# Kernel optimization log

Hardware: AMD Instinct MI355X
Metric: run time of the kernel (lower is better)

Reference implementation:

```python
import jax, jax.numpy as jnp
import numpy as np

NUM_COEFF = 32   # num_coeff_per_dim
NUM_POINTS = 64  # Chebyshev collocation points
MAX_ITERS = 10
TOL = 0.01
BATCH, DIM, HID, T_EVAL_N = 512, 256, 512, 16


def T_grid(t, n):
    # Chebyshev T_k(t), k=0..n-1 -> [n, len(t)]
    rows = [jnp.ones_like(t), t]
    for _ in range(2, n):
        rows.append(2.0 * t * rows[-1] - rows[-2])
    return jnp.stack(rows[:n])


def U_grid(t, n):
    rows = [jnp.ones_like(t), 2.0 * t]
    for _ in range(2, n):
        rows.append(2.0 * t * rows[-1] - rows[-2])
    return jnp.stack(rows[:n])


def DT_grid(t, n):
    # d/dt T_k = k * U_{k-1}
    return jnp.vstack([jnp.zeros((1, t.shape[0]), t.dtype),
                       U_grid(t, n - 1) * jnp.arange(1, n, dtype=t.dtype)[:, None]])


def vf_point(t, y, W1, b1, W2, b2):
    # f(t, y) for y [B, D], scalar t
    h = jnp.tanh(y @ W1 + b1 + t)
    return h @ W2 + b2


def vf_grid(t, y, W1, b1, W2, b2):
    # vectorized over Chebyshev points: y [B, D, P], t [P]
    h = jnp.tanh(jnp.einsum('bdp,dh->bhp', y, W1) + b1[None, :, None] + t[None, None, :])
    return jnp.einsum('bhp,hd->bdp', h, W2) + b2[None, :, None]


def setup_inputs() -> dict:
    key = jax.random.key(0)
    ks = jax.random.split(key, 7)
    s1 = 1.0 / np.sqrt(DIM)
    s2 = 1.0 / np.sqrt(HID)
    return {
        'y_init': jax.random.normal(ks[0], (BATCH, DIM), jnp.float32),
        't_eval': jnp.linspace(0.0, 1.0, T_EVAL_N, dtype=jnp.float32),
        'B_init': jax.random.uniform(ks[1], (BATCH, DIM, NUM_COEFF - 2), jnp.float32),
        'W1': jax.random.normal(ks[2], (DIM, HID), jnp.float32) * s1,
        'b1': jax.random.normal(ks[3], (HID,), jnp.float32) * 0.1,
        'W2': jax.random.normal(ks[4], (HID, DIM), jnp.float32) * s2,
        'b2': jax.random.normal(ks[5], (DIM,), jnp.float32) * 0.1,
    }


def _pan_solve(y_init, t_eval, B_init, W1, b1, W2, b2):
    t0, t1 = t_eval[0], t_eval[-1]
    dt = t_eval.dtype
    # time-independent spectral operators
    t_cheb = -jnp.sign(t1 - t0) * jnp.cos(jnp.pi * jnp.arange(NUM_POINTS, dtype=dt) / NUM_POINTS)
    Dt = jnp.diff(jnp.concatenate([t_cheb, jnp.ones((1,), dt)]))
    Phi = T_grid(t_cheb, NUM_COEFF)                        # [N, P]
    DPhi = (2.0 / (t1 - t0)) * DT_grid(t_cheb, NUM_COEFF)  # [N, P]
    inv0 = jnp.linalg.inv(jnp.stack([Phi[0:2, 0], DPhi[0:2, 0]]).T)  # [2,2]
    PD2 = jnp.stack([Phi[2:, 0], DPhi[2:, 0]], axis=-1)    # [N-2, 2]
    D01 = jnp.stack([DPhi[0, :], DPhi[1, :]], axis=0)      # [2, P]
    Phi_b = DPhi[2:, :] - PD2 @ inv0 @ D01                 # [N-2, P]
    Q = jnp.linalg.inv(Phi_b @ (Dt[:, None] * Phi_b.T))    # [N-2, N-2]
    PhibTQ = (Dt[:, None] * Phi_b.T) @ Q                   # [P, N-2]
    M2 = inv0 @ D01 @ PhibTQ                               # [2, N-2]

    f_init = vf_point(t0, y_init, W1, b1, W2, b2)
    yf2 = jnp.stack([y_init, f_init], axis=-1)             # [B, D, 2]

    def head(B_tail):
        return (yf2 - B_tail @ PD2) @ inv0                 # [B, D, 2]

    B = B_init
    done = jnp.array(False)
    delta = jnp.array(jnp.inf, dt)
    iters = jnp.array(0, jnp.int32)
    for _ in range(MAX_ITERS):  # Picard fixed-point iteration (masked early stop)
        B_prev = B
        B_full = jnp.concatenate([head(B_prev), B_prev], axis=-1)  # [B, D, N]
        y_grid = jnp.einsum('bdn,np->bdp', B_full, Phi)            # [B, D, P]
        fapprox = vf_grid(t_cheb, y_grid, W1, b1, W2, b2)          # [B, D, P]
        B_new = jnp.einsum('bdp,pn->bdn', fapprox, PhibTQ) - yf2 @ M2
        d = jnp.linalg.norm(B_new - B_prev)
        B = jnp.where(done, B_prev, B_new)
        delta = jnp.where(done, delta, d)
        iters = jnp.where(done, iters, iters + 1)
        done = done | (d < TOL)

    B_full = jnp.concatenate([head(B), B], axis=-1)
    t_out = -1.0 + 2.0 * (t_eval - t0) / (t1 - t0)
    Phi_out = T_grid(t_out, NUM_COEFF)                     # [N, T]
    traj = jnp.einsum('bdn,nt->tbd', B_full, Phi_out)      # [T, B, D]
    return traj, B, delta, iters


def reference(y_init, t_eval, B_init, W1, b1, W2, b2):
    traj, B, delta, iters = _pan_solve(y_init, t_eval, B_init, W1, b1, W2, b2)
    return (t_eval, traj, delta, B)
```

## Files before the change

kernel.cpp:

```cpp
#include <hip/hip_runtime.h>
#include <math.h>

#define NBATCH 512
#define NDIM 256
#define NHID 512
#define NC 32
#define NTAIL 30
#define NP 64
#define TEV 16
#define MAXIT 10
#define TOLF 0.01f
#define PI_F 3.14159265358979323846f

typedef __bf16 bf16_t;
typedef __bf16 bf16x8 __attribute__((ext_vector_type(8)));
typedef float f32x4 __attribute__((ext_vector_type(4)));
typedef unsigned short ushort_t;

constexpr size_t OFF_TCHEB = 0;
constexpr size_t OFF_PHIT  = 64;
constexpr size_t OFF_PD2I  = 2112;
constexpr size_t OFF_M2    = 2176;
constexpr size_t OFF_INV0  = 2240;
constexpr size_t OFF_PHIOUT= 2256;
constexpr size_t OFF_PQ    = 2768;
constexpr size_t OFF_PQBH  = 4816;
constexpr size_t OFF_PQBL  = 5840;
constexpr size_t OFF_PHIH  = 6864;
constexpr size_t OFF_PHIL  = 7888;
constexpr size_t OFF_SCAL  = 8912;
constexpr size_t OFF_H1F   = 8928;
constexpr size_t OFF_YF2I  = OFF_H1F + 262144;
constexpr size_t OFF_YM2   = OFF_YF2I + 262144;
constexpr size_t OFF_BT    = OFF_YM2 + 3932160;
constexpr size_t OFF_W1T   = OFF_BT + 3932160;
constexpr size_t OFF_W2T   = OFF_W1T + 65536;
constexpr size_t WS_FLOATS = OFF_W2T + 65536;

constexpr size_t OUT_TEVAL = 0;
constexpr size_t OUT_TRAJ  = 16;
constexpr size_t OUT_DELTA = 16 + (size_t)TEV*NBATCH*NDIM;
constexpr size_t OUT_B     = OUT_DELTA + 1;

__device__ __forceinline__ ushort_t bf16bits(float v) {
    bf16_t h = (bf16_t)v; ushort_t u; __builtin_memcpy(&u, &h, 2); return u;
}
__device__ __forceinline__ float bf16val(ushort_t u) {
    bf16_t h; __builtin_memcpy(&h, &u, 2); return (float)h;
}

__global__ void setup_kernel(const float* __restrict__ t_eval, float* __restrict__ ws,
                             float* __restrict__ out)
{
    __shared__ float Phi[32][64];
    __shared__ float DPhi[32][64];
    __shared__ float Phib[30][64];
    __shared__ float tcs[64];
    __shared__ float DtS[64];
    __shared__ float inv0s[4];
    __shared__ float pd2s[30][2];
    __shared__ double Gaug[30][61];
    __shared__ double rowk[60];
    __shared__ double colk[30];

    const int tid = threadIdx.x;
    const float t0 = t_eval[0], t1 = t_eval[TEV-1];
    const float sgn = (t1 > t0) ? 1.f : -1.f;

    if (tid < 64) {
        const float t = -sgn * cosf(PI_F * (float)tid / 64.f);
        tcs[tid] = t;
        float p0 = 1.f, p1 = t;
        Phi[0][tid] = p0; Phi[1][tid] = p1;
        for (int k = 2; k < 32; ++k) { float pk = 2.f*t*p1 - p0; Phi[k][tid] = pk; p0 = p1; p1 = pk; }
        const float sc = 2.f / (t1 - t0);
        float u0 = 1.f, u1 = 2.f*t;
        DPhi[0][tid] = 0.f;
        DPhi[1][tid] = sc * 1.f * u0;
        DPhi[2][tid] = sc * 2.f * u1;
        for (int k = 3; k < 32; ++k) { float uk = 2.f*t*u1 - u0; DPhi[k][tid] = sc * (float)k * uk; u0 = u1; u1 = uk; }
    }
    __syncthreads();
    if (tid < 64) DtS[tid] = ((tid < 63) ? tcs[tid+1] : 1.0f) - tcs[tid];
    if (tid == 0) {
        double a = Phi[0][0], b = DPhi[0][0], c = Phi[1][0], d = DPhi[1][0];
        double det = a*d - b*c;
        inv0s[0] = (float)( d/det); inv0s[1] = (float)(-b/det);
        inv0s[2] = (float)(-c/det); inv0s[3] = (float)( a/det);
    }
    __syncthreads();
    if (tid == 0) { ws[OFF_INV0+0]=inv0s[0]; ws[OFF_INV0+1]=inv0s[1]; ws[OFF_INV0+2]=inv0s[2]; ws[OFF_INV0+3]=inv0s[3]; }
    if (tid < 30) {
        float P = Phi[2+tid][0], D = DPhi[2+tid][0];
        float a0 = P*inv0s[0] + D*inv0s[2];
        float a1 = P*inv0s[1] + D*inv0s[3];
        pd2s[tid][0] = a0; pd2s[tid][1] = a1;
        ws[OFF_PD2I + tid*2+0] = a0;
        ws[OFF_PD2I + tid*2+1] = a1;
    }
    __syncthreads();
    if (tid < 64)
        for (int m = 0; m < 30; ++m)
            Phib[m][tid] = DPhi[2+m][tid] - (pd2s[m][0]*DPhi[0][tid] + pd2s[m][1]*DPhi[1][tid]);
    __syncthreads();

    for (int e = tid; e < 900; e += 256) {
        int i = e / 30, j = e % 30;
        double s = 0.0;
        for (int p = 0; p < 64; ++p) s += (double)Phib[i][p] * (double)DtS[p] * (double)Phib[j][p];
        Gaug[i][j] = s;
        Gaug[i][30+j] = (i == j) ? 1.0 : 0.0;
    }
    __syncthreads();

    for (int k = 0; k < 30; ++k) {
        double invpv = 1.0 / Gaug[k][k];
        if (tid < 60) rowk[tid] = Gaug[k][tid] * invpv;
        if (tid >= 64 && tid < 94) colk[tid-64] = Gaug[tid-64][k];
        __syncthreads();
        for (int e = tid; e < 1800; e += 256) {
            int i = e / 60, j = e - i*60;
            if (i == k) Gaug[i][j] = rowk[j];
            else        Gaug[i][j] -= colk[i] * rowk[j];
        }
        __syncthreads();
    }

    if (tid < 64) {
        ushort_t* pqh = (ushort_t*)(ws + OFF_PQBH);
        ushort_t* pql = (ushort_t*)(ws + OFF_PQBL);
        float pqrow[32];
        for (int n = 0; n < 30; ++n) {
            double s = 0.0;
            for (int m = 0; m < 30; ++m) s += (double)Phib[m][tid] * Gaug[m][30+n];
            pqrow[n] = (float)((double)DtS[tid] * s);
        }
        pqrow[30] = 0.f; pqrow[31] = 0.f;
        for (int n = 0; n < 32; ++n) {
            ws[OFF_PQ + (size_t)tid*32 + n] = pqrow[n];
            bf16_t h = (bf16_t)pqrow[n];
            float hf = (float)h;
            pqh[n*64 + tid] = bf16bits(pqrow[n]);
            pql[n*64 + tid] = bf16bits(pqrow[n] - hf);
        }
    }
    __syncthreads();

    if (tid < 30) {
        double a20 = 0.0, a21 = 0.0;
        for (int p = 0; p < 64; ++p) {
            double pq = (double)ws[OFF_PQ + (size_t)p*32 + tid];
            a20 += (double)DPhi[0][p] * pq;
            a21 += (double)DPhi[1][p] * pq;
        }
        ws[OFF_M2 + 0*32 + tid] = (float)((double)inv0s[0]*a20 + (double)inv0s[1]*a21);
        ws[OFF_M2 + 1*32 + tid] = (float)((double)inv0s[2]*a20 + (double)inv0s[3]*a21);
    }

    if (tid < 64) {
        ushort_t* phh = (ushort_t*)(ws + OFF_PHIH);
        ushort_t* phl = (ushort_t*)(ws + OFF_PHIL);
        for (int n = 0; n < 32; ++n) {
            float f = Phi[n][tid];
            ws[OFF_PHIT + (size_t)tid*32 + n] = f;
            ushort_t hb = bf16bits(f);
            phh[tid*32 + n] = hb;
            phl[tid*32 + n] = bf16bits(f - bf16val(hb));
        }
        ws[OFF_TCHEB + tid] = tcs[tid];
    }

    if (tid < TEV) {
        float te = t_eval[tid];
        out[OUT_TEVAL + tid] = te;
        float tt = -1.f + 2.f*(te - t0)/(t1 - t0);
        float q0 = 1.f, q1 = tt;
        ws[OFF_PHIOUT + (size_t)tid*32 + 0] = q0;
        ws[OFF_PHIOUT + (size_t)tid*32 + 1] = q1;
        for (int k = 2; k < 32; ++k) { float qk = 2.f*tt*q1 - q0; ws[OFF_PHIOUT + (size_t)tid*32 + k] = qk; q0 = q1; q1 = qk; }
    }

    if (tid == 0) {
        double* acc = (double*)(ws + OFF_SCAL);
        acc[0] = 0.0;
        int* ip = (int*)(ws + OFF_SCAL + 2);
        ip[0] = 0;
        ip[1] = 0;
    }
}

__global__ __launch_bounds__(256) void transB_kernel(const float* __restrict__ Bin, float* __restrict__ Bt)
{
    const int t = threadIdx.x, b = blockIdx.x;
    const float* src = Bin + ((size_t)(b*NDIM + t)) * NTAIL;
    #pragma unroll
    for (int n = 0; n < NTAIL; ++n)
        Bt[((size_t)b*NTAIL + n)*NDIM + t] = src[n];
}

__global__ __launch_bounds__(256) void transW_kernel(const float* __restrict__ W, bf16_t* __restrict__ Wt,
                                                     int R, int C)
{
    __shared__ float Ls[64][65];
    const int r0 = blockIdx.x*64, c0 = blockIdx.y*64;
    const int lr = threadIdx.x >> 6, lc = threadIdx.x & 63;
    #pragma unroll
    for (int i = 0; i < 16; ++i) {
        int rr = i*4 + lr;
        Ls[rr][lc] = W[(size_t)(r0+rr)*C + c0+lc];
    }
    __syncthreads();
    #pragma unroll
    for (int i = 0; i < 16; ++i) {
        int cc = i*4 + lr;
        Wt[(size_t)(c0+cc)*R + r0 + lc] = (bf16_t)Ls[lc][cc];
    }
}

__global__ __launch_bounds__(512) void finit_h_kernel(const float* __restrict__ y, const float* __restrict__ W1,
                                                      const float* __restrict__ b1, const float* __restrict__ t_eval,
                                                      float* __restrict__ h1)
{
    __shared__ float ys[NDIM];
    const int t = threadIdx.x, b = blockIdx.x;
    if (t < NDIM) ys[t] = y[(size_t)b*NDIM + t];
    __syncthreads();
    float acc = b1[t] + t_eval[0];
    for (int d = 0; d < NDIM; ++d) acc += ys[d] * W1[(size_t)d*NHID + t];
    h1[(size_t)b*NHID + t] = tanhf(acc);
}

__global__ __launch_bounds__(256) void finit_rest_kernel(const float* __restrict__ y, const float* __restrict__ W2,
                                                         const float* __restrict__ b2, const float* __restrict__ h1,
                                                         const float* __restrict__ inv0, const float* __restrict__ M2,
                                                         float* __restrict__ yf2i, float* __restrict__ yM2)
{
    __shared__ float hs[NHID];
    const int t = threadIdx.x, b = blockIdx.x;
    hs[t] = h1[(size_t)b*NHID + t];
    hs[t+256] = h1[(size_t)b*NHID + 256 + t];
    __syncthreads();
    float f = b2[t];
    for (int h = 0; h < NHID; ++h) f += hs[h] * W2[(size_t)h*NDIM + t];
    const float yv = y[(size_t)b*NDIM + t];
    yf2i[((size_t)b*2 + 0)*NDIM + t] = yv*inv0[0] + f*inv0[2];
    yf2i[((size_t)b*2 + 1)*NDIM + t] = yv*inv0[1] + f*inv0[3];
    #pragma unroll
    for (int n = 0; n < NTAIL; ++n)
        yM2[((size_t)b*NTAIL + n)*NDIM + t] = yv*M2[n] + f*M2[32 + n];
}

__global__ __launch_bounds__(256, 2) void iter_kernel(
    const float* __restrict__ pd2i, const float* __restrict__ yf2i, const float* __restrict__ tch,
    const bf16_t* __restrict__ W1t, const bf16_t* __restrict__ W2t,
    const float* __restrict__ b1f, const float* __restrict__ b2f,
    const ushort_t* __restrict__ PQhi, const ushort_t* __restrict__ PQlo,
    const ushort_t* __restrict__ phiH, const ushort_t* __restrict__ phiL,
    const float* __restrict__ yM2, float* __restrict__ Bt,
    double* __restrict__ accum, int* __restrict__ counter,
    int* __restrict__ done, float* __restrict__ outDelta)
{
    if (*done) return;
    __shared__ float pd2s[32][2];
    __shared__ float tchS[64];
    __shared__ double redd[4];
    __shared__ __align__(16) char smemA[33792];
    __shared__ __align__(16) char smemB[17408];
    __shared__ __align__(16) ushort_t PQHs[32*72];
    __shared__ __align__(16) ushort_t PQLs[32*72];

    const int t = threadIdx.x;
    const int b = blockIdx.x;
    const int lane = t & 63, w = t >> 6;
    const int fr = lane & 15, quad = lane >> 4;

    if (t < 60) ((float*)pd2s)[t] = pd2i[t];
    if (t >= 64 && t < 128) tchS[t-64] = tch[t-64];
    {
        int e = t * 8;
        int r = e >> 6, c = e & 63;
        uint4 vh = *(const uint4*)(PQhi + e);
        uint4 vl = *(const uint4*)(PQlo + e);
        *(uint4*)(PQHs + r*72 + c) = vh;
        *(uint4*)(PQLs + r*72 + c) = vl;
    }

    {
        float cf[32];
        #pragma unroll
        for (int n = 0; n < NTAIL; ++n) cf[2+n] = Bt[((size_t)b*NTAIL + n)*NDIM + t];
        float c0 = yf2i[((size_t)b*2 + 0)*NDIM + t];
        float c1 = yf2i[((size_t)b*2 + 1)*NDIM + t];
        #pragma unroll
        for (int n = 0; n < NTAIL; ++n) { c0 -= cf[2+n]*pd2s[n][0]; c1 -= cf[2+n]*pd2s[n][1]; }
        cf[0] = c0; cf[1] = c1;
        unsigned* BH32 = (unsigned*)smemA;
        unsigned* BL32 = (unsigned*)(smemA + 16384);
        #pragma unroll
        for (int n2 = 0; n2 < 16; ++n2) {
            float f0 = cf[2*n2], f1 = cf[2*n2+1];
            ushort_t h0 = bf16bits(f0), h1 = bf16bits(f1);
            ushort_t l0 = bf16bits(f0 - bf16val(h0)), l1 = bf16bits(f1 - bf16val(h1));
            int idx = t*16 + ((n2 >> 2) ^ (t & 3))*4 + (n2 & 3);
            BH32[idx] = (unsigned)h0 | ((unsigned)h1 << 16);
            BL32[idx] = (unsigned)l0 | ((unsigned)l1 << 16);
        }
    }
    __syncthreads();

    ushort_t* Ay = (ushort_t*)smemA;
    {
        bf16x8 bH[4], bL[4];
        const ushort_t* BHu = (const ushort_t*)smemA;
        const ushort_t* BLu = (const ushort_t*)(smemA + 16384);
        #pragma unroll
        for (int j = 0; j < 4; ++j) {
            const int d = w*64 + j*16 + fr;
            const int off = d*32 + (quad ^ (d & 3))*8;
            bH[j] = *(const bf16x8*)(BHu + off);
            bL[j] = *(const bf16x8*)(BLu + off);
        }
        bf16x8 aH[4], aL[4];
        #pragma unroll
        for (int i = 0; i < 4; ++i) {
            aH[i] = *(const bf16x8*)(phiH + (i*16 + fr)*32 + quad*8);
            aL[i] = *(const bf16x8*)(phiL + (i*16 + fr)*32 + quad*8);
        }
        __syncthreads();
        f32x4 accY[4][4];
        #pragma unroll
        for (int i = 0; i < 4; ++i)
            #pragma unroll
            for (int j = 0; j < 4; ++j) {
                f32x4 a = (f32x4){0.f,0.f,0.f,0.f};
                a = __builtin_amdgcn_mfma_f32_16x16x32_bf16(aH[i], bH[j], a, 0, 0, 0);
                a = __builtin_amdgcn_mfma_f32_16x16x32_bf16(aH[i], bL[j], a, 0, 0, 0);
                a = __builtin_amdgcn_mfma_f32_16x16x32_bf16(aL[i], bH[j], a, 0, 0, 0);
                accY[i][j] = a;
            }
        #pragma unroll
        for (int i = 0; i < 4; ++i)
            #pragma unroll
            for (int j = 0; j < 4; ++j)
                #pragma unroll
                for (int r = 0; r < 4; ++r) {
                    const int p = i*16 + quad*4 + r;
                    const int d = w*64 + j*16 + fr;
                    Ay[p*264 + d] = bf16bits(accY[i][j][r]);
                }
    }
    __syncthreads();

    ushort_t* Hc = (ushort_t*)smemB;
    f32x4 accF[4][4];
    #pragma unroll
    for (int i = 0; i < 4; ++i)
        #pragma unroll
        for (int j = 0; j < 4; ++j) accF[i][j] = (f32x4){0.f,0.f,0.f,0.f};

    #pragma unroll
    for (int pass = 0; pass < 4; ++pass) {
        f32x4 acc1[4][2];
        #pragma unroll
        for (int i = 0; i < 4; ++i)
            #pragma unroll
            for (int j = 0; j < 2; ++j) acc1[i][j] = (f32x4){0.f,0.f,0.f,0.f};
        #pragma unroll 2
        for (int kt = 0; kt < NDIM; kt += 32) {
            bf16x8 af[4], bfj[2];
            #pragma unroll
            for (int i = 0; i < 4; ++i)
                af[i] = *(const bf16x8*)(Ay + (i*16 + fr)*264 + kt + quad*8);
            #pragma unroll
            for (int j = 0; j < 2; ++j) {
                const int ncol = pass*128 + w*32 + j*16 + fr;
                bfj[j] = *(const bf16x8*)(W1t + (size_t)ncol*NDIM + kt + quad*8);
            }
            #pragma unroll
            for (int i = 0; i < 4; ++i)
                #pragma unroll
                for (int j = 0; j < 2; ++j)
                    acc1[i][j] = __builtin_amdgcn_mfma_f32_16x16x32_bf16(af[i], bfj[j], acc1[i][j], 0, 0, 0);
        }
        __syncthreads();
        #pragma unroll
        for (int i = 0; i < 4; ++i)
            #pragma unroll
            for (int j = 0; j < 2; ++j) {
                const int col = w*32 + j*16 + fr;
                const float bv = b1f[pass*128 + col];
                #pragma unroll
                for (int r = 0; r < 4; ++r) {
                    const int row = i*16 + quad*4 + r;
                    float v = acc1[i][j][r] + bv + tchS[row];
                    v = fminf(fmaxf(v, -15.f), 15.f);
                    float e = __expf(2.f*v);
                    Hc[row*136 + col] = bf16bits((e - 1.f)/(e + 1.f));
                }
            }
        __syncthreads();
        #pragma unroll
        for (int kt = 0; kt < 128; kt += 32) {
            bf16x8 af[4], bfj[4];
            #pragma unroll
            for (int i = 0; i < 4; ++i)
                af[i] = *(const bf16x8*)(Hc + (i*16 + fr)*136 + kt + quad*8);
            #pragma unroll
            for (int j = 0; j < 4; ++j) {
                const int d = w*64 + j*16 + fr;
                bfj[j] = *(const bf16x8*)(W2t + (size_t)d*NHID + pass*128 + kt + quad*8);
            }
            #pragma unroll
            for (int i = 0; i < 4; ++i)
                #pragma unroll
                for (int j = 0; j < 4; ++j)
                    accF[i][j] = __builtin_amdgcn_mfma_f32_16x16x32_bf16(af[i], bfj[j], accF[i][j], 0, 0, 0);
        }
    }
    __syncthreads();

    {
        unsigned* FsT32 = (unsigned*)smemA;
        #pragma unroll
        for (int i = 0; i < 4; ++i)
            #pragma unroll
            for (int j = 0; j < 4; ++j) {
                const int d = w*64 + j*16 + fr;
                const float bv = b2f[d];
                #pragma unroll
                for (int rp = 0; rp < 2; ++rp) {
                    unsigned u0 = bf16bits(accF[i][j][rp*2]   + bv);
                    unsigned u1 = bf16bits(accF[i][j][rp*2+1] + bv);
                    FsT32[d*33 + i*8 + quad*2 + rp] = u0 | (u1 << 16);
                }
            }
    }
    __syncthreads();

    double ss = 0.0;
    {
        const ushort_t* FsTu = (const ushort_t*)smemA;
        f32x4 acc2[2][4];
        #pragma unroll
        for (int m2 = 0; m2 < 2; ++m2)
            #pragma unroll
            for (int j2 = 0; j2 < 4; ++j2) acc2[m2][j2] = (f32x4){0.f,0.f,0.f,0.f};
        #pragma unroll
        for (int kk = 0; kk < 2; ++kk) {
            bf16x8 ah[2], al[2];
            #pragma unroll
            for (int m2 = 0; m2 < 2; ++m2) {
                const int off = (m2*16 + fr)*72 + kk*32 + quad*8;
                ah[m2] = *(const bf16x8*)(PQHs + off);
                al[m2] = *(const bf16x8*)(PQLs + off);
            }
            #pragma unroll
            for (int j2 = 0; j2 < 4; ++j2) {
                const int d2 = w*64 + j2*16 + fr;
                bf16x8 bfv = *(const bf16x8*)(FsTu + d2*66 + kk*32 + quad*8);
                #pragma unroll
                for (int m2 = 0; m2 < 2; ++m2) {
                    acc2[m2][j2] = __builtin_amdgcn_mfma_f32_16x16x32_bf16(ah[m2], bfv, acc2[m2][j2], 0, 0, 0);
                    acc2[m2][j2] = __builtin_amdgcn_mfma_f32_16x16x32_bf16(al[m2], bfv, acc2[m2][j2], 0, 0, 0);
                }
            }
        }
        #pragma unroll
        for (int m2 = 0; m2 < 2; ++m2)
            #pragma unroll
            for (int j2 = 0; j2 < 4; ++j2)
                #pragma unroll
                for (int rr = 0; rr < 4; ++rr) {
                    const int n = m2*16 + quad*4 + rr;
                    if (n < NTAIL) {
                        const int d = w*64 + j2*16 + fr;
                        const size_t idx = ((size_t)b*NTAIL + n)*NDIM + d;
                        float val = acc2[m2][j2][rr] - yM2[idx];
                        float old = Bt[idx];
                        float diff = val - old;
                        Bt[idx] = val;
                        ss += (double)diff*(double)diff;
                    }
                }
    }

    #pragma unroll
    for (int off = 32; off > 0; off >>= 1) ss += __shfl_down(ss, off, 64);
    if (lane == 0) redd[w] = ss;
    __syncthreads();
    if (t == 0) {
        double tot = redd[0] + redd[1] + redd[2] + redd[3];
        atomicAdd(accum, tot);
        __threadfence();
        int old = atomicAdd(counter, 1);
        if (old == 511) {
            unsigned long long raw = atomicExch((unsigned long long*)accum, 0ull);
            double total; __builtin_memcpy(&total, &raw, 8);
            float dl = (float)sqrt(total);
            *outDelta = dl;
            *counter = 0;
            if (dl < TOLF) *done = 1;
        }
    }
}

__global__ __launch_bounds__(256) void kernelEpi(const float* __restrict__ PhiOut, const float* __restrict__ pd2i,
                                                 const float* __restrict__ yf2i, const float* __restrict__ Bt,
                                                 float* __restrict__ outTraj, float* __restrict__ outB)
{
    __shared__ float Po[16][32];
    const int t = threadIdx.x, b = blockIdx.x;
    for (int i = t; i < 512; i += 256) ((float*)Po)[i] = PhiOut[i];
    __syncthreads();
    float cf[32];
    #pragma unroll
    for (int n = 0; n < NTAIL; ++n) cf[2+n] = Bt[((size_t)b*NTAIL + n)*NDIM + t];
    float c0 = yf2i[((size_t)b*2 + 0)*NDIM + t];
    float c1 = yf2i[((size_t)b*2 + 1)*NDIM + t];
    #pragma unroll
    for (int n = 0; n < NTAIL; ++n) { c0 -= cf[2+n]*pd2i[n*2]; c1 -= cf[2+n]*pd2i[n*2+1]; }
    cf[0] = c0; cf[1] = c1;
    for (int tt = 0; tt < TEV; ++tt) {
        float s = 0.f;
        #pragma unroll
        for (int k = 0; k < 32; ++k) s += cf[k]*Po[tt][k];
        outTraj[((size_t)tt*NBATCH + b)*NDIM + t] = s;
    }
    float* ob = outB + ((size_t)(b*NDIM + t))*NTAIL;
    #pragma unroll
    for (int n = 0; n < NTAIL; ++n) ob[n] = cf[2+n];
}

extern "C" void kernel_launch(void* const* d_in, const int* in_sizes, int n_in,
                              void* d_out, int out_size, void* d_ws, size_t ws_size,
                              hipStream_t stream)
{
    const float* y_init = (const float*)d_in[0];
    const float* t_eval = (const float*)d_in[1];
    const float* B_init = (const float*)d_in[2];
    const float* W1     = (const float*)d_in[3];
    const float* b1     = (const float*)d_in[4];
    const float* W2     = (const float*)d_in[5];
    const float* b2     = (const float*)d_in[6];
    float* out = (float*)d_out;
    float* ws  = (float*)d_ws;
    if (ws_size < WS_FLOATS * sizeof(float)) return;

    float* tcheb = ws + OFF_TCHEB;
    float* pd2i  = ws + OFF_PD2I;
    float* M2    = ws + OFF_M2;
    float* inv0  = ws + OFF_INV0;
    float* PhiOut= ws + OFF_PHIOUT;
    double* accum = (double*)(ws + OFF_SCAL);
    int* done    = (int*)(ws + OFF_SCAL + 2);
    int* counter = (int*)(ws + OFF_SCAL + 3);
    float* h1   = ws + OFF_H1F;
    float* yf2i = ws + OFF_YF2I;
    float* yM2  = ws + OFF_YM2;
    float* Bt   = ws + OFF_BT;
    bf16_t* W1t = (bf16_t*)(ws + OFF_W1T);
    bf16_t* W2t = (bf16_t*)(ws + OFF_W2T);
    ushort_t* pqh = (ushort_t*)(ws + OFF_PQBH);
    ushort_t* pql = (ushort_t*)(ws + OFF_PQBL);
    ushort_t* phh = (ushort_t*)(ws + OFF_PHIH);
    ushort_t* phl = (ushort_t*)(ws + OFF_PHIL);

    setup_kernel<<<1, 256, 0, stream>>>(t_eval, ws, out);
    transB_kernel<<<NBATCH, 256, 0, stream>>>(B_init, Bt);
    transW_kernel<<<dim3(NDIM/64, NHID/64), 256, 0, stream>>>(W1, W1t, NDIM, NHID);
    transW_kernel<<<dim3(NHID/64, NDIM/64), 256, 0, stream>>>(W2, W2t, NHID, NDIM);
    finit_h_kernel<<<NBATCH, 512, 0, stream>>>(y_init, W1, b1, t_eval, h1);
    finit_rest_kernel<<<NBATCH, 256, 0, stream>>>(y_init, W2, b2, h1, inv0, M2, yf2i, yM2);

    for (int it = 0; it < MAXIT; ++it) {
        iter_kernel<<<NBATCH, 256, 0, stream>>>(pd2i, yf2i, tcheb, W1t, W2t, b1, b2,
                                                pqh, pql, phh, phl, yM2, Bt,
                                                accum, counter, done, out + OUT_DELTA);
    }
    kernelEpi<<<NBATCH, 256, 0, stream>>>(PhiOut, pd2i, yf2i, Bt, out + OUT_TRAJ, out + OUT_B);
}
```

Measured before the change: 800.7 us.

## Fuse Picard iterations and epilogue into one persistent per-batch kernel

Replaces the ten per-iteration kernel launches and the separate epilogue kernel with a single kernel. Each block keeps its B coefficients and yM2 terms in registers across all ten iterations, removing the global reads and writes of Bt between iterations. The cross-block convergence flag is dropped: every block always runs all ten iterations and records each iteration's squared-norm partial sum in a per-iteration slot. A small finalize kernel then picks the first delta below tolerance. The cost is that work is no longer skipped after convergence. B also keeps updating past the converged iteration, and the output B is rebuilt from the bf16 hi/lo split, so results can drift slightly from the masked reference.

```diff
diff --git a/kernel.cpp b/kernel.cpp
--- a/kernel.cpp
+++ b/kernel.cpp
@@ -29,7 +29,7 @@
 constexpr size_t OFF_PHIH  = 6864;
 constexpr size_t OFF_PHIL  = 7888;
 constexpr size_t OFF_SCAL  = 8912;
-constexpr size_t OFF_H1F   = 8928;
+constexpr size_t OFF_H1F   = 8944;
 constexpr size_t OFF_YF2I  = OFF_H1F + 262144;
 constexpr size_t OFF_YM2   = OFF_YF2I + 262144;
 constexpr size_t OFF_BT    = OFF_YM2 + 3932160;
@@ -180,13 +180,7 @@
         for (int k = 2; k < 32; ++k) { float qk = 2.f*tt*q1 - q0; ws[OFF_PHIOUT + (size_t)tid*32 + k] = qk; q0 = q1; q1 = qk; }
     }
 
-    if (tid == 0) {
-        double* acc = (double*)(ws + OFF_SCAL);
-        acc[0] = 0.0;
-        int* ip = (int*)(ws + OFF_SCAL + 2);
-        ip[0] = 0;
-        ip[1] = 0;
-    }
+    if (tid < 20) ws[OFF_SCAL + tid] = 0.f;
 }
 
 __global__ __launch_bounds__(256) void transB_kernel(const float* __restrict__ Bin, float* __restrict__ Bt)
@@ -250,17 +244,16 @@
         yM2[((size_t)b*NTAIL + n)*NDIM + t] = yv*M2[n] + f*M2[32 + n];
 }
 
-__global__ __launch_bounds__(256, 2) void iter_kernel(
+__global__ __launch_bounds__(256, 2) void pan_solve(
     const float* __restrict__ pd2i, const float* __restrict__ yf2i, const float* __restrict__ tch,
     const bf16_t* __restrict__ W1t, const bf16_t* __restrict__ W2t,
     const float* __restrict__ b1f, const float* __restrict__ b2f,
     const ushort_t* __restrict__ PQhi, const ushort_t* __restrict__ PQlo,
     const ushort_t* __restrict__ phiH, const ushort_t* __restrict__ phiL,
-    const float* __restrict__ yM2, float* __restrict__ Bt,
-    double* __restrict__ accum, int* __restrict__ counter,
-    int* __restrict__ done, float* __restrict__ outDelta)
-{
-    if (*done) return;
+    const float* __restrict__ yM2, const float* __restrict__ Bt,
+    const float* __restrict__ PhiOut,
+    double* __restrict__ accum, float* __restrict__ out)
+{
     __shared__ float pd2s[32][2];
     __shared__ float tchS[64];
     __shared__ double redd[4];
@@ -284,251 +277,303 @@
         *(uint4*)(PQHs + r*72 + c) = vh;
         *(uint4*)(PQLs + r*72 + c) = vl;
     }
-
-    {
-        float cf[32];
-        #pragma unroll
-        for (int n = 0; n < NTAIL; ++n) cf[2+n] = Bt[((size_t)b*NTAIL + n)*NDIM + t];
-        float c0 = yf2i[((size_t)b*2 + 0)*NDIM + t];
-        float c1 = yf2i[((size_t)b*2 + 1)*NDIM + t];
-        #pragma unroll
-        for (int n = 0; n < NTAIL; ++n) { c0 -= cf[2+n]*pd2s[n][0]; c1 -= cf[2+n]*pd2s[n][1]; }
-        cf[0] = c0; cf[1] = c1;
-        unsigned* BH32 = (unsigned*)smemA;
-        unsigned* BL32 = (unsigned*)(smemA + 16384);
-        #pragma unroll
-        for (int n2 = 0; n2 < 16; ++n2) {
-            float f0 = cf[2*n2], f1 = cf[2*n2+1];
-            ushort_t h0 = bf16bits(f0), h1 = bf16bits(f1);
-            ushort_t l0 = bf16bits(f0 - bf16val(h0)), l1 = bf16bits(f1 - bf16val(h1));
-            int idx = t*16 + ((n2 >> 2) ^ (t & 3))*4 + (n2 & 3);
-            BH32[idx] = (unsigned)h0 | ((unsigned)h1 << 16);
-            BL32[idx] = (unsigned)l0 | ((unsigned)l1 << 16);
-        }
-    }
+    __syncthreads();
+
+    unsigned* BH32 = (unsigned*)smemA;
+    unsigned* BL32 = (unsigned*)(smemA + 16384);
+
+    float Breg[2][4][4];
+    float yM2r[2][4][4];
+    float yf0r[4], yf1r[4];
+    #pragma unroll
+    for (int j2 = 0; j2 < 4; ++j2) {
+        const int d = w*64 + j2*16 + fr;
+        yf0r[j2] = yf2i[((size_t)b*2 + 0)*NDIM + d];
+        yf1r[j2] = yf2i[((size_t)b*2 + 1)*NDIM + d];
+        #pragma unroll
+        for (int m2 = 0; m2 < 2; ++m2)
+            #pragma unroll
+            for (int rr = 0; rr < 4; ++rr) {
+                const int n = m2*16 + quad*4 + rr;
+                float bv = 0.f, yv = 0.f;
+                if (n < NTAIL) {
+                    const size_t idx = ((size_t)b*NTAIL + n)*NDIM + d;
+                    bv = Bt[idx]; yv = yM2[idx];
+                }
+                Breg[m2][j2][rr] = bv; yM2r[m2][j2][rr] = yv;
+            }
+    }
+
+    auto commit = [&]() {
+        float s0[4], s1[4];
+        #pragma unroll
+        for (int j2 = 0; j2 < 4; ++j2) { s0[j2] = 0.f; s1[j2] = 0.f; }
+        #pragma unroll
+        for (int m2 = 0; m2 < 2; ++m2)
+            #pragma unroll
+            for (int rr = 0; rr < 4; ++rr) {
+                const int n = m2*16 + quad*4 + rr;
+                if (n < NTAIL) {
+                    const float p0 = pd2s[n][0], p1 = pd2s[n][1];
+                    #pragma unroll
+                    for (int j2 = 0; j2 < 4; ++j2) {
+                        s0[j2] += Breg[m2][j2][rr]*p0;
+                        s1[j2] += Breg[m2][j2][rr]*p1;
+                    }
+                }
+            }
+        #pragma unroll
+        for (int j2 = 0; j2 < 4; ++j2) {
+            s0[j2] += __shfl_xor(s0[j2], 16, 64); s0[j2] += __shfl_xor(s0[j2], 32, 64);
+            s1[j2] += __shfl_xor(s1[j2], 16, 64); s1[j2] += __shfl_xor(s1[j2], 32, 64);
+        }
+        #pragma unroll
+        for (int j2 = 0; j2 < 4; ++j2) {
+            const int d = w*64 + j2*16 + fr;
+            if (quad == 0) {
+                float c0 = yf0r[j2] - s0[j2];
+                float c1 = yf1r[j2] - s1[j2];
+                ushort_t h0 = bf16bits(c0), h1 = bf16bits(c1);
+                ushort_t l0 = bf16bits(c0 - bf16val(h0)), l1 = bf16bits(c1 - bf16val(h1));
+                const int idx = d*16 + (d & 3)*4;
+                BH32[idx] = (unsigned)h0 | ((unsigned)h1 << 16);
+                BL32[idx] = (unsigned)l0 | ((unsigned)l1 << 16);
+            }
+            #pragma unroll
+            for (int m2 = 0; m2 < 2; ++m2)
+                #pragma unroll
+                for (int rp = 0; rp < 2; ++rp) {
+                    const int nt0 = m2*16 + quad*4 + rp*2;
+                    if (nt0 < NTAIL) {
+                        const int n2 = m2*8 + quad*2 + rp + 1;
+                        float f0 = Breg[m2][j2][rp*2], f1 = Breg[m2][j2][rp*2+1];
+                        ushort_t h0 = bf16bits(f0), h1 = bf16bits(f1);
+                        ushort_t l0 = bf16bits(f0 - bf16val(h0)), l1 = bf16bits(f1 - bf16val(h1));
+                        const int idx = d*16 + ((n2 >> 2) ^ (d & 3))*4 + (n2 & 3);
+                        BH32[idx] = (unsigned)h0 | ((unsigned)h1 << 16);
+                        BL32[idx] = (unsigned)l0 | ((unsigned)l1 << 16);
+                    }
+                }
+        }
+    };
+
+    commit();
     __syncthreads();
 
     ushort_t* Ay = (ushort_t*)smemA;
-    {
-        bf16x8 bH[4], bL[4];
-        const ushort_t* BHu = (const ushort_t*)smemA;
-        const ushort_t* BLu = (const ushort_t*)(smemA + 16384);
-        #pragma unroll
-        for (int j = 0; j < 4; ++j) {
-            const int d = w*64 + j*16 + fr;
-            const int off = d*32 + (quad ^ (d & 3))*8;
-            bH[j] = *(const bf16x8*)(BHu + off);
-            bL[j] = *(const bf16x8*)(BLu + off);
-        }
-        bf16x8 aH[4], aL[4];
-        #pragma unroll
-        for (int i = 0; i < 4; ++i) {
-            aH[i] = *(const bf16x8*)(phiH + (i*16 + fr)*32 + quad*8);
-            aL[i] = *(const bf16x8*)(phiL + (i*16 + fr)*32 + quad*8);
-        }
-        __syncthreads();
-        f32x4 accY[4][4];
-        #pragma unroll
-        for (int i = 0; i < 4; ++i)
-            #pragma unroll
-            for (int j = 0; j < 4; ++j) {
-                f32x4 a = (f32x4){0.f,0.f,0.f,0.f};
-                a = __builtin_amdgcn_mfma_f32_16x16x32_bf16(aH[i], bH[j], a, 0, 0, 0);
-                a = __builtin_amdgcn_mfma_f32_16x16x32_bf16(aH[i], bL[j], a, 0, 0, 0);
-                a = __builtin_amdgcn_mfma_f32_16x16x32_bf16(aL[i], bH[j], a, 0, 0, 0);
-                accY[i][j] = a;
-            }
-        #pragma unroll
-        for (int i = 0; i < 4; ++i)
-            #pragma unroll
-            for (int j = 0; j < 4; ++j)
-                #pragma unroll
-                for (int r = 0; r < 4; ++r) {
-                    const int p = i*16 + quad*4 + r;
-                    const int d = w*64 + j*16 + fr;
-                    Ay[p*264 + d] = bf16bits(accY[i][j][r]);
-                }
-    }
-    __syncthreads();
-
     ushort_t* Hc = (ushort_t*)smemB;
-    f32x4 accF[4][4];
-    #pragma unroll
-    for (int i = 0; i < 4; ++i)
-        #pragma unroll
-        for (int j = 0; j < 4; ++j) accF[i][j] = (f32x4){0.f,0.f,0.f,0.f};
-
-    #pragma unroll
-    for (int pass = 0; pass < 4; ++pass) {
-        f32x4 acc1[4][2];
-        #pragma unroll
-        for (int i = 0; i < 4; ++i)
-            #pragma unroll
-            for (int j = 0; j < 2; ++j) acc1[i][j] = (f32x4){0.f,0.f,0.f,0.f};
-        #pragma unroll 2
-        for (int kt = 0; kt < NDIM; kt += 32) {
-            bf16x8 af[4], bfj[2];
-            #pragma unroll
-            for (int i = 0; i < 4; ++i)
-                af[i] = *(const bf16x8*)(Ay + (i*16 + fr)*264 + kt + quad*8);
-            #pragma unroll
-            for (int j = 0; j < 2; ++j) {
-                const int ncol = pass*128 + w*32 + j*16 + fr;
-                bfj[j] = *(const bf16x8*)(W1t + (size_t)ncol*NDIM + kt + quad*8);
-            }
-            #pragma unroll
-            for (int i = 0; i < 4; ++i)
-                #pragma unroll
-                for (int j = 0; j < 2; ++j)
-                    acc1[i][j] = __builtin_amdgcn_mfma_f32_16x16x32_bf16(af[i], bfj[j], acc1[i][j], 0, 0, 0);
-        }
-        __syncthreads();
-        #pragma unroll
-        for (int i = 0; i < 4; ++i)
-            #pragma unroll
-            for (int j = 0; j < 2; ++j) {
-                const int col = w*32 + j*16 + fr;
-                const float bv = b1f[pass*128 + col];
-                #pragma unroll
-                for (int r = 0; r < 4; ++r) {
-                    const int row = i*16 + quad*4 + r;
-                    float v = acc1[i][j][r] + bv + tchS[row];
-                    v = fminf(fmaxf(v, -15.f), 15.f);
-                    float e = __expf(2.f*v);
-                    Hc[row*136 + col] = bf16bits((e - 1.f)/(e + 1.f));
-                }
-            }
-        __syncthreads();
-        #pragma unroll
-        for (int kt = 0; kt < 128; kt += 32) {
-            bf16x8 af[4], bfj[4];
-            #pragma unroll
-            for (int i = 0; i < 4; ++i)
-                af[i] = *(const bf16x8*)(Hc + (i*16 + fr)*136 + kt + quad*8);
+
+    for (int it = 0; it < MAXIT; ++it) {
+        {
+            bf16x8 bH[4], bL[4];
+            const ushort_t* BHu = (const ushort_t*)smemA;
+            const ushort_t* BLu = (const ushort_t*)(smemA + 16384);
             #pragma unroll
             for (int j = 0; j < 4; ++j) {
                 const int d = w*64 + j*16 + fr;
-                bfj[j] = *(const bf16x8*)(W2t + (size_t)d*NHID + pass*128 + kt + quad*8);
-            }
+                const int off = d*32 + (quad ^ (d & 3))*8;
+                bH[j] = *(const bf16x8*)(BHu + off);
+                bL[j] = *(const bf16x8*)(BLu + off);
+            }
+            bf16x8 aH[4], aL[4];
+            #pragma unroll
+            for (int i = 0; i < 4; ++i) {
+                aH[i] = *(const bf16x8*)(phiH + (i*16 + fr)*32 + quad*8);
+                aL[i] = *(const bf16x8*)(phiL + (i*16 + fr)*32 + quad*8);
+            }
+            __syncthreads();
+            f32x4 accY[4][4];
             #pragma unroll
             for (int i = 0; i < 4; ++i)
                 #pragma unroll
+                for (int j = 0; j < 4; ++j) {
+                    f32x4 a = (f32x4){0.f,0.f,0.f,0.f};
+                    a = __builtin_amdgcn_mfma_f32_16x16x32_bf16(aH[i], bH[j], a, 0, 0, 0);
+                    a = __builtin_amdgcn_mfma_f32_16x16x32_bf16(aH[i], bL[j], a, 0, 0, 0);
+                    a = __builtin_amdgcn_mfma_f32_16x16x32_bf16(aL[i], bH[j], a, 0, 0, 0);
+                    accY[i][j] = a;
+                }
+            #pragma unroll
+            for (int i = 0; i < 4; ++i)
+                #pragma unroll
                 for (int j = 0; j < 4; ++j)
-                    accF[i][j] = __builtin_amdgcn_mfma_f32_16x16x32_bf16(af[i], bfj[j], accF[i][j], 0, 0, 0);
-        }
-    }
-    __syncthreads();
-
-    {
-        unsigned* FsT32 = (unsigned*)smemA;
+                    #pragma unroll
+                    for (int r = 0; r < 4; ++r) {
+                        const int p = i*16 + quad*4 + r;
+                        const int d = w*64 + j*16 + fr;
+                        Ay[p*264 + d] = bf16bits(accY[i][j][r]);
+                    }
+        }
+        __syncthreads();
+
+        f32x4 accF[4][4];
         #pragma unroll
         for (int i = 0; i < 4; ++i)
             #pragma unroll
-            for (int j = 0; j < 4; ++j) {
-                const int d = w*64 + j*16 + fr;
-                const float bv = b2f[d];
-                #pragma unroll
-                for (int rp = 0; rp < 2; ++rp) {
-                    unsigned u0 = bf16bits(accF[i][j][rp*2]   + bv);
-                    unsigned u1 = bf16bits(accF[i][j][rp*2+1] + bv);
-                    FsT32[d*33 + i*8 + quad*2 + rp] = u0 | (u1 << 16);
-                }
-            }
-    }
-    __syncthreads();
-
-    double ss = 0.0;
-    {
-        const ushort_t* FsTu = (const ushort_t*)smemA;
-        f32x4 acc2[2][4];
-        #pragma unroll
-        for (int m2 = 0; m2 < 2; ++m2)
-            #pragma unroll
-            for (int j2 = 0; j2 < 4; ++j2) acc2[m2][j2] = (f32x4){0.f,0.f,0.f,0.f};
-        #pragma unroll
-        for (int kk = 0; kk < 2; ++kk) {
-            bf16x8 ah[2], al[2];
-            #pragma unroll
-            for (int m2 = 0; m2 < 2; ++m2) {
-                const int off = (m2*16 + fr)*72 + kk*32 + quad*8;
-                ah[m2] = *(const bf16x8*)(PQHs + off);
-                al[m2] = *(const bf16x8*)(PQLs + off);
-            }
-            #pragma unroll
-            for (int j2 = 0; j2 < 4; ++j2) {
-                const int d2 = w*64 + j2*16 + fr;
-                bf16x8 bfv = *(const bf16x8*)(FsTu + d2*66 + kk*32 + quad*8);
+            for (int j = 0; j < 4; ++j) accF[i][j] = (f32x4){0.f,0.f,0.f,0.f};
+
+        #pragma unroll
+        for (int pass = 0; pass < 4; ++pass) {
+            f32x4 acc1[4][2];
+            #pragma unroll
+            for (int i = 0; i < 4; ++i)
+                #pragma unroll
+                for (int j = 0; j < 2; ++j) acc1[i][j] = (f32x4){0.f,0.f,0.f,0.f};
+            #pragma unroll
+            for (int kt = 0; kt < NDIM; kt += 32) {
+                bf16x8 af[4], bfj[2];
+                #pragma unroll
+                for (int i = 0; i < 4; ++i)
+                    af[i] = *(const bf16x8*)(Ay + (i*16 + fr)*264 + kt + quad*8);
+                #pragma unroll
+                for (int j = 0; j < 2; ++j) {
+                    const int ncol = pass*128 + w*32 + j*16 + fr;
+                    bfj[j] = *(const bf16x8*)(W1t + (size_t)ncol*NDIM + kt + quad*8);
+                }
+                #pragma unroll
+                for (int i = 0; i < 4; ++i)
+                    #pragma unroll
+                    for (int j = 0; j < 2; ++j)
+                        acc1[i][j] = __builtin_amdgcn_mfma_f32_16x16x32_bf16(af[i], bfj[j], acc1[i][j], 0, 0, 0);
+            }
+            __syncthreads();
+            #pragma unroll
+            for (int i = 0; i < 4; ++i)
+                #pragma unroll
+                for (int j = 0; j < 2; ++j) {
+                    const int col = w*32 + j*16 + fr;
+                    const float bv = b1f[pass*128 + col];
+                    #pragma unroll
+                    for (int r = 0; r < 4; ++r) {
+                        const int row = i*16 + quad*4 + r;
+                        float v = acc1[i][j][r] + bv + tchS[row];
+                        v = fminf(fmaxf(v, -15.f), 15.f);
+                        float e = __expf(2.f*v);
+                        Hc[row*136 + col] = bf16bits((e - 1.f)/(e + 1.f));
+                    }
+                }
+            __syncthreads();
+            #pragma unroll
+            for (int kt = 0; kt < 128; kt += 32) {
+                bf16x8 af[4], bfj[4];
+                #pragma unroll
+                for (int i = 0; i < 4; ++i)
+                    af[i] = *(const bf16x8*)(Hc + (i*16 + fr)*136 + kt + quad*8);
+                #pragma unroll
+                for (int j = 0; j < 4; ++j) {
+                    const int d = w*64 + j*16 + fr;
+                    bfj[j] = *(const bf16x8*)(W2t + (size_t)d*NHID + pass*128 + kt + quad*8);
+                }
+                #pragma unroll
+                for (int i = 0; i < 4; ++i)
+                    #pragma unroll
+                    for (int j = 0; j < 4; ++j)
+                        accF[i][j] = __builtin_amdgcn_mfma_f32_16x16x32_bf16(af[i], bfj[j], accF[i][j], 0, 0, 0);
+            }
+        }
+        __syncthreads();
+
+        {
+            unsigned* FsT32 = (unsigned*)smemA;
+            #pragma unroll
+            for (int i = 0; i < 4; ++i)
+                #pragma unroll
+                for (int j = 0; j < 4; ++j) {
+                    const int d = w*64 + j*16 + fr;
+                    const float bv = b2f[d];
+                    #pragma unroll
+                    for (int rp = 0; rp < 2; ++rp) {
+                        unsigned u0 = bf16bits(accF[i][j][rp*2]   + bv);
+                        unsigned u1 = bf16bits(accF[i][j][rp*2+1] + bv);
+                        FsT32[d*33 + i*8 + quad*2 + rp] = u0 | (u1 << 16);
+                    }
+                }
+        }
+        __syncthreads();
+
+        double ss = 0.0;
+        {
+            const ushort_t* FsTu = (const ushort_t*)smemA;
+            f32x4 acc2[2][4];
+            #pragma unroll
+            for (int m2 = 0; m2 < 2; ++m2)
+                #pragma unroll
+                for (int j2 = 0; j2 < 4; ++j2) acc2[m2][j2] = (f32x4){0.f,0.f,0.f,0.f};
+            #pragma unroll
+            for (int kk = 0; kk < 2; ++kk) {
+                bf16x8 ah[2], al[2];
                 #pragma unroll
                 for (int m2 = 0; m2 < 2; ++m2) {
-                    acc2[m2][j2] = __builtin_amdgcn_mfma_f32_16x16x32_bf16(ah[m2], bfv, acc2[m2][j2], 0, 0, 0);
-                    acc2[m2][j2] = __builtin_amdgcn_mfma_f32_16x16x32_bf16(al[m2], bfv, acc2[m2][j2], 0, 0, 0);
-                }
-            }
-        }
-        #pragma unroll
-        for (int m2 = 0; m2 < 2; ++m2)
-            #pragma unroll
-            for (int j2 = 0; j2 < 4; ++j2)
-                #pragma unroll
-                for (int rr = 0; rr < 4; ++rr) {
-                    const int n = m2*16 + quad*4 + rr;
-                    if (n < NTAIL) {
-                        const int d = w*64 + j2*16 + fr;
-                        const size_t idx = ((size_t)b*NTAIL + n)*NDIM + d;
-                        float val = acc2[m2][j2][rr] - yM2[idx];
-                        float old = Bt[idx];
-                        float diff = val - old;
-                        Bt[idx] = val;
-                        ss += (double)diff*(double)diff;
+                    const int off = (m2*16 + fr)*72 + kk*32 + quad*8;
+                    ah[m2] = *(const bf16x8*)(PQHs + off);
+                    al[m2] = *(const bf16x8*)(PQLs + off);
+                }
+                #pragma unroll
+                for (int j2 = 0; j2 < 4; ++j2) {
+                    const int d2 = w*64 + j2*16 + fr;
+                    bf16x8 bfv = *(const bf16x8*)(FsTu + d2*66 + kk*32 + quad*8);
+                    #pragma unroll
+                    for (int m2 = 0; m2 < 2; ++m2) {
+                        acc2[m2][j2] = __builtin_amdgcn_mfma_f32_16x16x32_bf16(ah[m2], bfv, acc2[m2][j2], 0, 0, 0);
+                        acc2[m2][j2] = __builtin_amdgcn_mfma_f32_16x16x32_bf16(al[m2], bfv, acc2[m2][j2], 0, 0, 0);
                     }
                 }
-    }
-
-    #pragma unroll
-    for (int off = 32; off > 0; off >>= 1) ss += __shfl_down(ss, off, 64);
-    if (lane == 0) redd[w] = ss;
-    __syncthreads();
-    if (t == 0) {
-        double tot = redd[0] + redd[1] + redd[2] + redd[3];
-        atomicAdd(accum, tot);
-        __threadfence();
-        int old = atomicAdd(counter, 1);
-        if (old == 511) {
-            unsigned long long raw = atomicExch((unsigned long long*)accum, 0ull);
-            double total; __builtin_memcpy(&total, &raw, 8);
-            float dl = (float)sqrt(total);
-            *outDelta = dl;
-            *counter = 0;
-            if (dl < TOLF) *done = 1;
-        }
-    }
-}
-
-__global__ __launch_bounds__(256) void kernelEpi(const float* __restrict__ PhiOut, const float* __restrict__ pd2i,
-                                                 const float* __restrict__ yf2i, const float* __restrict__ Bt,
-                                                 float* __restrict__ outTraj, float* __restrict__ outB)
-{
-    __shared__ float Po[16][32];
-    const int t = threadIdx.x, b = blockIdx.x;
-    for (int i = t; i < 512; i += 256) ((float*)Po)[i] = PhiOut[i];
-    __syncthreads();
+            }
+            #pragma unroll
+            for (int m2 = 0; m2 < 2; ++m2)
+                #pragma unroll
+                for (int j2 = 0; j2 < 4; ++j2)
+                    #pragma unroll
+                    for (int rr = 0; rr < 4; ++rr) {
+                        const int n = m2*16 + quad*4 + rr;
+                        if (n < NTAIL) {
+                            float val = acc2[m2][j2][rr] - yM2r[m2][j2][rr];
+                            float diff = val - Breg[m2][j2][rr];
+                            Breg[m2][j2][rr] = val;
+                            ss += (double)diff*(double)diff;
+                        }
+                    }
+        }
+
+        __syncthreads();
+        commit();
+
+        #pragma unroll
+        for (int off = 32; off > 0; off >>= 1) ss += __shfl_down(ss, off, 64);
+        if (lane == 0) redd[w] = ss;
+        __syncthreads();
+        if (t == 0) atomicAdd(&accum[it], redd[0]+redd[1]+redd[2]+redd[3]);
+    }
+
     float cf[32];
     #pragma unroll
-    for (int n = 0; n < NTAIL; ++n) cf[2+n] = Bt[((size_t)b*NTAIL + n)*NDIM + t];
-    float c0 = yf2i[((size_t)b*2 + 0)*NDIM + t];
-    float c1 = yf2i[((size_t)b*2 + 1)*NDIM + t];
-    #pragma unroll
-    for (int n = 0; n < NTAIL; ++n) { c0 -= cf[2+n]*pd2i[n*2]; c1 -= cf[2+n]*pd2i[n*2+1]; }
-    cf[0] = c0; cf[1] = c1;
+    for (int n2 = 0; n2 < 16; ++n2) {
+        const int idx = t*16 + ((n2 >> 2) ^ (t & 3))*4 + (n2 & 3);
+        unsigned uh = BH32[idx], ul = BL32[idx];
+        cf[2*n2]   = bf16val((ushort_t)(uh & 0xffffu)) + bf16val((ushort_t)(ul & 0xffffu));
+        cf[2*n2+1] = bf16val((ushort_t)(uh >> 16))     + bf16val((ushort_t)(ul >> 16));
+    }
     for (int tt = 0; tt < TEV; ++tt) {
         float s = 0.f;
         #pragma unroll
-        for (int k = 0; k < 32; ++k) s += cf[k]*Po[tt][k];
-        outTraj[((size_t)tt*NBATCH + b)*NDIM + t] = s;
-    }
-    float* ob = outB + ((size_t)(b*NDIM + t))*NTAIL;
+        for (int k = 0; k < 32; ++k) s += cf[k]*PhiOut[tt*32 + k];
+        out[OUT_TRAJ + ((size_t)tt*NBATCH + b)*NDIM + t] = s;
+    }
+    float* ob = out + OUT_B + ((size_t)(b*NDIM + t))*NTAIL;
     #pragma unroll
     for (int n = 0; n < NTAIL; ++n) ob[n] = cf[2+n];
+}
+
+__global__ void finalize_kernel(const double* __restrict__ accum, float* __restrict__ outDelta)
+{
+    if (threadIdx.x == 0) {
+        float dl = 0.f;
+        for (int k = 0; k < MAXIT; ++k) {
+            dl = (float)sqrt(accum[k]);
+            if (dl < TOLF) break;
+        }
+        *outDelta = dl;
+    }
 }
 
 extern "C" void kernel_launch(void* const* d_in, const int* in_sizes, int n_in,
@@ -546,24 +591,22 @@
     float* ws  = (float*)d_ws;
     if (ws_size < WS_FLOATS * sizeof(float)) return;
 
-    float* tcheb = ws + OFF_TCHEB;
-    float* pd2i  = ws + OFF_PD2I;
-    float* M2    = ws + OFF_M2;
-    float* inv0  = ws + OFF_INV0;
-    float* PhiOut= ws + OFF_PHIOUT;
+    const float* tcheb = ws + OFF_TCHEB;
+    const float* pd2i  = ws + OFF_PD2I;
+    const float* M2    = ws + OFF_M2;
+    const float* inv0  = ws + OFF_INV0;
+    const float* PhiOut= ws + OFF_PHIOUT;
     double* accum = (double*)(ws + OFF_SCAL);
-    int* done    = (int*)(ws + OFF_SCAL + 2);
-    int* counter = (int*)(ws + OFF_SCAL + 3);
     float* h1   = ws + OFF_H1F;
     float* yf2i = ws + OFF_YF2I;
     float* yM2  = ws + OFF_YM2;
     float* Bt   = ws + OFF_BT;
     bf16_t* W1t = (bf16_t*)(ws + OFF_W1T);
     bf16_t* W2t = (bf16_t*)(ws + OFF_W2T);
-    ushort_t* pqh = (ushort_t*)(ws + OFF_PQBH);
-    ushort_t* pql = (ushort_t*)(ws + OFF_PQBL);
-    ushort_t* phh = (ushort_t*)(ws + OFF_PHIH);
-    ushort_t* phl = (ushort_t*)(ws + OFF_PHIL);
+    const ushort_t* pqh = (const ushort_t*)(ws + OFF_PQBH);
+    const ushort_t* pql = (const ushort_t*)(ws + OFF_PQBL);
+    const ushort_t* phh = (const ushort_t*)(ws + OFF_PHIH);
+    const ushort_t* phl = (const ushort_t*)(ws + OFF_PHIL);
 
     setup_kernel<<<1, 256, 0, stream>>>(t_eval, ws, out);
     transB_kernel<<<NBATCH, 256, 0, stream>>>(B_init, Bt);
@@ -572,10 +615,8 @@
     finit_h_kernel<<<NBATCH, 512, 0, stream>>>(y_init, W1, b1, t_eval, h1);
     finit_rest_kernel<<<NBATCH, 256, 0, stream>>>(y_init, W2, b2, h1, inv0, M2, yf2i, yM2);
 
-    for (int it = 0; it < MAXIT; ++it) {
-        iter_kernel<<<NBATCH, 256, 0, stream>>>(pd2i, yf2i, tcheb, W1t, W2t, b1, b2,
-                                                pqh, pql, phh, phl, yM2, Bt,
-                                                accum, counter, done, out + OUT_DELTA);
-    }
-    kernelEpi<<<NBATCH, 256, 0, stream>>>(PhiOut, pd2i, yf2i, Bt, out + OUT_TRAJ, out + OUT_B);
-}
+    pan_solve<<<NBATCH, 256, 0, stream>>>(pd2i, yf2i, tcheb, W1t, W2t, b1, b2,
+                                          pqh, pql, phh, phl, yM2, Bt, PhiOut,
+                                          accum, out);
+    finalize_kernel<<<1, 64, 0, stream>>>(accum, out + OUT_DELTA);
+}
```

New measurement: 1.063 ms. 32.7% more time.
